# Performance work log

Measured on AMD Instinct MI355X. Metric: run time of the kernel, lower is better.

The kernel has to match this reference:

```python
import jax, jax.numpy as jnp
import numpy as np

T, H, E, I, SI, TOP_K = 4096, 2048, 16, 1024, 4096, 1


def setup_inputs() -> dict:
    key = jax.random.key(0)
    ks = jax.random.split(key, 8)
    s_h = 1.0 / np.sqrt(H)
    s_i = 1.0 / np.sqrt(I)
    s_si = 1.0 / np.sqrt(SI)
    return {
        "hidden_states": jax.random.normal(ks[0], (T, H), jnp.float32),
        "router_w": jax.random.normal(ks[1], (E, H), jnp.float32) * s_h,
        "w_gate": jax.random.normal(ks[2], (E, H, I), jnp.float32) * s_h,
        "w_up": jax.random.normal(ks[3], (E, H, I), jnp.float32) * s_h,
        "w_down": jax.random.normal(ks[4], (E, I, H), jnp.float32) * s_i,
        "ws_gate": jax.random.normal(ks[5], (H, SI), jnp.float32) * s_h,
        "ws_up": jax.random.normal(ks[6], (H, SI), jnp.float32) * s_h,
        "ws_down": jax.random.normal(ks[7], (SI, H), jnp.float32) * s_si,
    }


def reference(hidden_states, router_w, w_gate, w_up, w_down, ws_gate, ws_up, ws_down):
    x = hidden_states  # [T, H]
    # Router: logits -> top-k -> sigmoid weights (Llama4RenormalizeMoeRoutingMethod)
    logits = jnp.einsum("th,eh->te", x, router_w)              # [T, E]
    top_vals, top_idx = jax.lax.top_k(logits, TOP_K)            # [T, K]
    weights = jax.nn.sigmoid(top_vals)                          # [T, K]
    # dispatch[t, e] = router weight if expert e selected for token t, else 0
    onehot = jax.nn.one_hot(top_idx, E, dtype=x.dtype)          # [T, K, E]
    dispatch = jnp.einsum("tke,tk->te", onehot, weights)        # [T, E]
    # Routed experts: router weight applied on input (commutes through the
    # linear gate/up projections as a per-(t,e) scalar applied before SiLU).
    g = jnp.einsum("th,ehi->tei", x, w_gate) * dispatch[:, :, None]  # [T, E, I]
    u = jnp.einsum("th,ehi->tei", x, w_up) * dispatch[:, :, None]    # [T, E, I]
    act = jax.nn.silu(g) * u                                          # [T, E, I]
    # Unselected experts contribute exactly 0 (act==0 there), so summing over
    # E in the down projection is the combine step.
    routed = jnp.einsum("tei,eih->th", act, w_down)             # [T, H]
    # Shared expert (SiLU-gated MLP on the unscaled hidden states)
    shared = (jax.nn.silu(x @ ws_gate) * (x @ ws_up)) @ ws_down  # [T, H]
    return shared + routed
```

## Files before the change

kernel.cpp:

```cpp
#include <hip/hip_runtime.h>
#include <hip/hip_bf16.h>

typedef unsigned short u16;
typedef unsigned int   u32;
typedef __attribute__((ext_vector_type(8))) short short8;
typedef __attribute__((ext_vector_type(4))) float f32x4;

#define T_TOK 4096
#define HDIM  2048
#define NEXP  16
#define IDIM  1024
#define SIDIM 4096
#define RCAP  6144
#define NTIL  48

#define O_WT      0u
#define O_EIDX    16384u
#define O_CNT     32768u
#define O_POS     32832u
#define O_PADOFF  32896u
#define O_TILEEXP 33024u
#define O_TOKROW  33280u
#define O_XBF     65536u
#define O_XSC     (O_XBF + 2u*T_TOK*HDIM)
#define O_ACTS    (O_XSC + 2u*RCAP*HDIM)
#define O_ACTR    (O_ACTS + 2u*T_TOK*SIDIM)

__device__ __forceinline__ u16 f2b(float f) {
  u32 u = __float_as_uint(f);
  u = (u + 0x7FFFu + ((u >> 16) & 1u)) >> 16;
  return (u16)u;
}

__global__ __launch_bounds__(256) void router_k(
    const float* __restrict__ x, const float* __restrict__ rw,
    float* __restrict__ wt, int* __restrict__ eidx, int* __restrict__ cnt) {
  int w = threadIdx.x >> 6, l = threadIdx.x & 63;
  int t = blockIdx.x * 4 + w;
  double acc[NEXP];
#pragma unroll
  for (int e = 0; e < NEXP; ++e) acc[e] = 0.0;
  const float* xp = x + (size_t)t * HDIM;
  for (int hb = 0; hb < HDIM; hb += 256) {
    float4 xv = *(const float4*)(xp + hb + l * 4);
#pragma unroll
    for (int e = 0; e < NEXP; ++e) {
      float4 wv = *(const float4*)(rw + (size_t)e * HDIM + hb + l * 4);
      acc[e] += (double)xv.x * wv.x + (double)xv.y * wv.y
              + (double)xv.z * wv.z + (double)xv.w * wv.w;
    }
  }
#pragma unroll
  for (int e = 0; e < NEXP; ++e) {
    double v = acc[e];
#pragma unroll
    for (int off = 32; off; off >>= 1) v += __shfl_xor(v, off, 64);
    acc[e] = v;
  }
  if (l == 0) {
    double best = acc[0]; int be = 0;
#pragma unroll
    for (int e = 1; e < NEXP; ++e) if (acc[e] > best) { best = acc[e]; be = e; }
    wt[t] = 1.0f / (1.0f + __expf(-(float)best));
    eidx[t] = be;
    atomicAdd(&cnt[be], 1);
  }
}

__global__ void scan_k(const int* __restrict__ cnt, int* __restrict__ pad_off,
                       int* __restrict__ tile_exp, int* __restrict__ pos,
                       int* __restrict__ tok_row) {
  if (threadIdx.x == 0) {
    for (int i = 0; i < 64; ++i) tile_exp[i] = -1;
    int run = 0;
    for (int e = 0; e < NEXP; ++e) {
      pad_off[e] = run;
      int pc = ((cnt[e] + 127) >> 7) << 7;
      for (int tt = run >> 7; tt < (run + pc) >> 7; ++tt) tile_exp[tt] = e;
      run += pc;
      pos[e] = 0;
    }
    pad_off[NEXP] = run;
  }
  for (int i = threadIdx.x; i < RCAP; i += 256) tok_row[i] = -1;
}

__global__ void assign_k(const int* __restrict__ eidx, const int* __restrict__ pad_off,
                         int* __restrict__ pos, int* __restrict__ tok_row) {
  int t = blockIdx.x * 256 + threadIdx.x;
  if (t >= T_TOK) return;
  int e = eidx[t];
  int r = atomicAdd(&pos[e], 1);
  tok_row[pad_off[e] + r] = t;
}

__global__ __launch_bounds__(256) void cvt_k(
    const float* __restrict__ x, const float* __restrict__ wt,
    const int* __restrict__ tok_row, u16* __restrict__ xbf, u16* __restrict__ xsc) {
  int row = blockIdx.x;
  int tid = threadIdx.x;
  if (row < T_TOK) {
    const float* src = x + (size_t)row * HDIM;
    u16* dst = xbf + (size_t)row * HDIM;
#pragma unroll
    for (int i = 0; i < 2; ++i) {
      int c = i * 1024 + tid * 4;
      float4 v = *(const float4*)(src + c);
      uint2 o;
      o.x = (u32)f2b(v.x) | ((u32)f2b(v.y) << 16);
      o.y = (u32)f2b(v.z) | ((u32)f2b(v.w) << 16);
      *(uint2*)(dst + c) = o;
    }
  } else {
    int g = row - T_TOK;
    u16* dst = xsc + (size_t)g * HDIM;
    int t = tok_row[g];
    if (t < 0) {
      uint2 z; z.x = 0u; z.y = 0u;
#pragma unroll
      for (int i = 0; i < 2; ++i) *(uint2*)(dst + i * 1024 + tid * 4) = z;
    } else {
      float s = wt[t];
      const float* src = x + (size_t)t * HDIM;
#pragma unroll
      for (int i = 0; i < 2; ++i) {
        int c = i * 1024 + tid * 4;
        float4 v = *(const float4*)(src + c);
        uint2 o;
        o.x = (u32)f2b(v.x * s) | ((u32)f2b(v.y * s) << 16);
        o.y = (u32)f2b(v.z * s) | ((u32)f2b(v.w * s) << 16);
        *(uint2*)(dst + c) = o;
      }
    }
  }
}


template<bool ROUTED>
__global__ __launch_bounds__(256) void gemm_gu(
    const u16* __restrict__ A, int lda,
    const float* __restrict__ Bg0, const float* __restrict__ Bu0, int ldb,
    int K, u16* __restrict__ act, int ldact,
    const int* __restrict__ tile_exp) {
  __shared__ __align__(16) u16 As[128 * 64];
  __shared__ __align__(16) u16 Bgs[64 * 72];
  __shared__ __align__(16) u16 Bus[64 * 72];
  const int tid = threadIdx.x;
  const int w = tid >> 6, l = tid & 63;
  const int wm = w >> 1, wn = w & 1;
  const int m0 = blockIdx.y * 128, n0 = blockIdx.x * 64;
  const float* Bg = Bg0;
  const float* Bu = Bu0;
  if (ROUTED) {
    int e = tile_exp[blockIdx.y];
    if (e < 0) return;
    size_t off = (size_t)e * (size_t)K * (size_t)ldb;
    Bg += off; Bu += off;
  }
  f32x4 accg[4][2], accu[4][2];
#pragma unroll
  for (int i = 0; i < 4; ++i)
#pragma unroll
    for (int j = 0; j < 2; ++j)
#pragma unroll
      for (int r = 0; r < 4; ++r) { accg[i][j][r] = 0.0f; accu[i][j][r] = 0.0f; }

  const int ra = tid >> 3;
  const int ca = (tid & 7) * 8;
  const u16* Ab = A + (size_t)m0 * lda;

  for (int k0 = 0; k0 < K; k0 += 64) {
    __syncthreads();
#pragma unroll
    for (int i = 0; i < 4; ++i) {
      int r = ra + 32 * i;
      int4 v = *(const int4*)(Ab + (size_t)r * lda + k0 + ca);
      *(int4*)&As[r * 64 + (ca ^ ((r & 7) * 8))] = v;
    }
    {
      const float* bp = Bg + (size_t)(k0 + w * 16) * ldb + n0 + l;
      u16 h[16];
#pragma unroll
      for (int i = 0; i < 16; ++i) h[i] = f2b(bp[(size_t)i * ldb]);
#pragma unroll
      for (int j = 0; j < 4; ++j) {
        uint2 v; v.x = (u32)h[4*j] | ((u32)h[4*j+1] << 16);
        v.y = (u32)h[4*j+2] | ((u32)h[4*j+3] << 16);
        *(uint2*)&Bgs[l * 72 + w * 16 + j * 4] = v;
      }
      bp = Bu + (size_t)(k0 + w * 16) * ldb + n0 + l;
#pragma unroll
      for (int i = 0; i < 16; ++i) h[i] = f2b(bp[(size_t)i * ldb]);
#pragma unroll
      for (int j = 0; j < 4; ++j) {
        uint2 v; v.x = (u32)h[4*j] | ((u32)h[4*j+1] << 16);
        v.y = (u32)h[4*j+2] | ((u32)h[4*j+3] << 16);
        *(uint2*)&Bus[l * 72 + w * 16 + j * 4] = v;
      }
    }
    __syncthreads();
#pragma unroll
    for (int kh = 0; kh < 2; ++kh) {
      short8 af[4];
#pragma unroll
      for (int mf = 0; mf < 4; ++mf) {
        int r = wm * 64 + mf * 16 + (l & 15);
        int c = (kh * 32 + (l >> 4) * 8) ^ ((r & 7) * 8);
        af[mf] = *(const short8*)&As[r * 64 + c];
      }
      short8 bgf[2], buf2[2];
#pragma unroll
      for (int nf = 0; nf < 2; ++nf) {
        int n = wn * 32 + nf * 16 + (l & 15);
        int c = kh * 32 + (l >> 4) * 8;
        bgf[nf]  = *(const short8*)&Bgs[n * 72 + c];
        buf2[nf] = *(const short8*)&Bus[n * 72 + c];
      }
#pragma unroll
      for (int mf = 0; mf < 4; ++mf)
#pragma unroll
        for (int nf = 0; nf < 2; ++nf) {
          accg[mf][nf] = __builtin_amdgcn_mfma_f32_16x16x32_bf16(af[mf], bgf[nf],  accg[mf][nf], 0, 0, 0);
          accu[mf][nf] = __builtin_amdgcn_mfma_f32_16x16x32_bf16(af[mf], buf2[nf], accu[mf][nf], 0, 0, 0);
        }
    }
  }
#pragma unroll
  for (int mf = 0; mf < 4; ++mf)
#pragma unroll
    for (int nf = 0; nf < 2; ++nf) {
      int col = n0 + wn * 32 + nf * 16 + (l & 15);
#pragma unroll
      for (int r = 0; r < 4; ++r) {
        int row = m0 + wm * 64 + mf * 16 + (l >> 4) * 4 + r;
        float g = accg[mf][nf][r], u = accu[mf][nf][r];
        float s = g / (1.0f + __expf(-g));
        act[(size_t)row * ldact + col] = f2b(s * u);
      }
    }
}

template<bool ROUTED>
__global__ __launch_bounds__(256) void gemm_down(
    const u16* __restrict__ A, int lda,
    const float* __restrict__ B0, int ldb, int K,
    float* __restrict__ out, int ldout,
    const int* __restrict__ tile_exp, const int* __restrict__ tok_row) {
  __shared__ __align__(16) u16 As[128 * 64];
  __shared__ __align__(16) u16 Bs[64 * 72];
  const int tid = threadIdx.x;
  const int w = tid >> 6, l = tid & 63;
  const int wm = w >> 1, wn = w & 1;
  const int m0 = blockIdx.y * 128, n0 = blockIdx.x * 64;
  const float* B = B0;
  if (ROUTED) {
    int e = tile_exp[blockIdx.y];
    if (e < 0) return;
    B += (size_t)e * (size_t)K * (size_t)ldb;
  }
  f32x4 acc[4][2];
#pragma unroll
  for (int i = 0; i < 4; ++i)
#pragma unroll
    for (int j = 0; j < 2; ++j)
#pragma unroll
      for (int r = 0; r < 4; ++r) acc[i][j][r] = 0.0f;

  const int ra = tid >> 3;
  const int ca = (tid & 7) * 8;
  const u16* Ab = A + (size_t)m0 * lda;

  for (int k0 = 0; k0 < K; k0 += 64) {
    __syncthreads();
#pragma unroll
    for (int i = 0; i < 4; ++i) {
      int r = ra + 32 * i;
      int4 v = *(const int4*)(Ab + (size_t)r * lda + k0 + ca);
      *(int4*)&As[r * 64 + (ca ^ ((r & 7) * 8))] = v;
    }
    {
      const float* bp = B + (size_t)(k0 + w * 16) * ldb + n0 + l;
      u16 h[16];
#pragma unroll
      for (int i = 0; i < 16; ++i) h[i] = f2b(bp[(size_t)i * ldb]);
#pragma unroll
      for (int j = 0; j < 4; ++j) {
        uint2 v; v.x = (u32)h[4*j] | ((u32)h[4*j+1] << 16);
        v.y = (u32)h[4*j+2] | ((u32)h[4*j+3] << 16);
        *(uint2*)&Bs[l * 72 + w * 16 + j * 4] = v;
      }
    }
    __syncthreads();
#pragma unroll
    for (int kh = 0; kh < 2; ++kh) {
      short8 af[4];
#pragma unroll
      for (int mf = 0; mf < 4; ++mf) {
        int r = wm * 64 + mf * 16 + (l & 15);
        int c = (kh * 32 + (l >> 4) * 8) ^ ((r & 7) * 8);
        af[mf] = *(const short8*)&As[r * 64 + c];
      }
      short8 bf[2];
#pragma unroll
      for (int nf = 0; nf < 2; ++nf) {
        int n = wn * 32 + nf * 16 + (l & 15);
        int c = kh * 32 + (l >> 4) * 8;
        bf[nf] = *(const short8*)&Bs[n * 72 + c];
      }
#pragma unroll
      for (int mf = 0; mf < 4; ++mf)
#pragma unroll
        for (int nf = 0; nf < 2; ++nf)
          acc[mf][nf] = __builtin_amdgcn_mfma_f32_16x16x32_bf16(af[mf], bf[nf], acc[mf][nf], 0, 0, 0);
    }
  }
#pragma unroll
  for (int mf = 0; mf < 4; ++mf)
#pragma unroll
    for (int nf = 0; nf < 2; ++nf) {
      int col = n0 + wn * 32 + nf * 16 + (l & 15);
#pragma unroll
      for (int r = 0; r < 4; ++r) {
        int grow = m0 + wm * 64 + mf * 16 + (l >> 4) * 4 + r;
        float v = acc[mf][nf][r];
        if (ROUTED) {
          int t = tok_row[grow];
          if (t >= 0) out[(size_t)t * ldout + col] += v;
        } else {
          out[(size_t)grow * ldout + col] = v;
        }
      }
    }
}

extern "C" void kernel_launch(void* const* d_in, const int* in_sizes, int n_in,
                              void* d_out, int out_size, void* d_ws, size_t ws_size,
                              hipStream_t stream) {
  const float* x   = (const float*)d_in[0];
  const float* rw  = (const float*)d_in[1];
  const float* wg  = (const float*)d_in[2];
  const float* wu  = (const float*)d_in[3];
  const float* wd  = (const float*)d_in[4];
  const float* wsg = (const float*)d_in[5];
  const float* wsu = (const float*)d_in[6];
  const float* wsd = (const float*)d_in[7];
  float* out = (float*)d_out;
  char* ws = (char*)d_ws;

  float* wt     = (float*)(ws + O_WT);
  int* eidx     = (int*)(ws + O_EIDX);
  int* cnt      = (int*)(ws + O_CNT);
  int* pos      = (int*)(ws + O_POS);
  int* pad_off  = (int*)(ws + O_PADOFF);
  int* tile_exp = (int*)(ws + O_TILEEXP);
  int* tok_row  = (int*)(ws + O_TOKROW);
  u16* xbf      = (u16*)(ws + O_XBF);
  u16* xsc      = (u16*)(ws + O_XSC);
  u16* acts     = (u16*)(ws + O_ACTS);
  u16* actr     = (u16*)(ws + O_ACTR);

  hipMemsetAsync(ws + O_CNT, 0, 128, stream);
  router_k<<<T_TOK / 4, 256, 0, stream>>>(x, rw, wt, eidx, cnt);
  scan_k<<<1, 256, 0, stream>>>(cnt, pad_off, tile_exp, pos, tok_row);
  assign_k<<<T_TOK / 256, 256, 0, stream>>>(eidx, pad_off, pos, tok_row);
  cvt_k<<<T_TOK + RCAP, 256, 0, stream>>>(x, wt, tok_row, xbf, xsc);
  gemm_gu<false><<<dim3(SIDIM / 64, T_TOK / 128), 256, 0, stream>>>(
      xbf, HDIM, wsg, wsu, SIDIM, HDIM, acts, SIDIM, nullptr);
  gemm_gu<true><<<dim3(IDIM / 64, NTIL), 256, 0, stream>>>(
      xsc, HDIM, wg, wu, IDIM, HDIM, actr, IDIM, tile_exp);
  gemm_down<false><<<dim3(HDIM / 64, T_TOK / 128), 256, 0, stream>>>(
      acts, SIDIM, wsd, HDIM, SIDIM, out, HDIM, nullptr, nullptr);
  gemm_down<true><<<dim3(HDIM / 64, NTIL), 256, 0, stream>>>(
      actr, IDIM, wd, HDIM, IDIM, out, HDIM, tile_exp, tok_row);
}
```

Before: 630.5 us.

## Pre-transpose weights to bf16 and rewrite GEMMs with async LDS pipelining

Adds a transpose-convert kernel that turns every fp32 weight matrix into a K-contiguous bf16 copy in workspace on each call. The GEMMs then fetch A and B straight into LDS with global_load_lds and 16-byte loads instead of strided fp32 loads converted in registers. The shared-expert GEMMs move to new 512-thread kernels with 256x128 tiles, double-buffered LDS, barrier-interleaved prefetch, s_setprio around the MFMAs and block-index swizzling. The routed GEMMs use the transposed weights, and the routed down projection gets wider tiles. In exchange, every call re-reads and rewrites all weights, which is extra memory traffic.

After: 649.0 us. 1.03x slower.

```diff
diff --git a/kernel.cpp b/kernel.cpp
--- a/kernel.cpp
+++ b/kernel.cpp
@@ -22,15 +22,28 @@
 #define O_TILEEXP 33024u
 #define O_TOKROW  33280u
 #define O_XBF     65536u
-#define O_XSC     (O_XBF + 2u*T_TOK*HDIM)
-#define O_ACTS    (O_XSC + 2u*RCAP*HDIM)
+#define O_XSC     (O_XBF  + 2u*T_TOK*HDIM)
+#define O_ACTS    (O_XSC  + 2u*RCAP*HDIM)
 #define O_ACTR    (O_ACTS + 2u*T_TOK*SIDIM)
+#define O_WSGT    (O_ACTR + 2u*RCAP*IDIM)
+#define O_WSUT    (O_WSGT + 2u*SIDIM*HDIM)
+#define O_WSDT    (O_WSUT + 2u*SIDIM*HDIM)
+#define O_WGT     (O_WSDT + 2u*HDIM*SIDIM)
+#define O_WUT     (O_WGT  + 2u*NEXP*IDIM*HDIM)
+#define O_WDT     (O_WUT  + 2u*NEXP*IDIM*HDIM)
 
 __device__ __forceinline__ u16 f2b(float f) {
   u32 u = __float_as_uint(f);
   u = (u + 0x7FFFu + ((u >> 16) & 1u)) >> 16;
   return (u16)u;
 }
+
+#define GLDS16(g, l) __builtin_amdgcn_global_load_lds( \
+    (const __attribute__((address_space(1))) void*)(g), \
+    (__attribute__((address_space(3))) void*)(l), 16, 0, 0)
+#define BARX() __builtin_amdgcn_s_barrier()
+#define SETPRIO(x) __builtin_amdgcn_s_setprio(x)
+#define WAITVM(n) asm volatile("s_waitcnt vmcnt(" #n ")" ::: "memory")
 
 __global__ __launch_bounds__(256) void router_k(
     const float* __restrict__ x, const float* __restrict__ rw,
@@ -135,28 +148,243 @@
   }
 }
 
-
-template<bool ROUTED>
-__global__ __launch_bounds__(256) void gemm_gu(
-    const u16* __restrict__ A, int lda,
-    const float* __restrict__ Bg0, const float* __restrict__ Bu0, int ldb,
-    int K, u16* __restrict__ act, int ldact,
-    const int* __restrict__ tile_exp) {
+__global__ __launch_bounds__(256) void tconv_k(
+    const float* __restrict__ src, u16* __restrict__ dst, int K, int N) {
+  __shared__ u32 lt[64][36];
+  size_t boff = (size_t)blockIdx.z * (size_t)K * N;
+  const int n0 = blockIdx.x * 64, k0 = blockIdx.y * 64;
+  const int l = threadIdx.x & 63, w = threadIdx.x >> 6;
+  const float* sp = src + boff + (size_t)(k0 + w * 16) * N + n0 + l;
+  u32 p[8];
+#pragma unroll
+  for (int i = 0; i < 8; ++i) {
+    float a = sp[(size_t)(2 * i) * N];
+    float b = sp[(size_t)(2 * i + 1) * N];
+    p[i] = (u32)f2b(a) | ((u32)f2b(b) << 16);
+  }
+  *(uint4*)&lt[l][w * 8 + 0] = make_uint4(p[0], p[1], p[2], p[3]);
+  *(uint4*)&lt[l][w * 8 + 4] = make_uint4(p[4], p[5], p[6], p[7]);
+  __syncthreads();
+  const int c = threadIdx.x & 7, n2 = threadIdx.x >> 3;
+#pragma unroll
+  for (int rnd = 0; rnd < 2; ++rnd) {
+    int n = n2 + rnd * 32;
+    uint4 v = *(const uint4*)&lt[n][c * 4];
+    *(uint4*)(dst + boff + (size_t)(n0 + n) * K + k0 + c * 8) = v;
+  }
+}
+
+
+__device__ __forceinline__ void mmA(f32x4 (&acc)[4][8], const short8 (&af)[4],
+                                    const short8 (&bfr)[4], int h) {
+  SETPRIO(1);
+#pragma unroll
+  for (int mf = 0; mf < 4; ++mf)
+#pragma unroll
+    for (int nf = 0; nf < 4; ++nf)
+      acc[mf][h * 4 + nf] = __builtin_amdgcn_mfma_f32_16x16x32_bf16(
+          af[mf], bfr[nf], acc[mf][h * 4 + nf], 0, 0, 0);
+  SETPRIO(0);
+}
+__device__ __forceinline__ void mmD(f32x4 (&acc)[4][4], const short8 (&af)[4],
+                                    const short8 (&bfr)[2], int h) {
+  SETPRIO(1);
+#pragma unroll
+  for (int mf = 0; mf < 4; ++mf)
+#pragma unroll
+    for (int nf = 0; nf < 2; ++nf)
+      acc[mf][h * 2 + nf] = __builtin_amdgcn_mfma_f32_16x16x32_bf16(
+          af[mf], bfr[nf], acc[mf][h * 2 + nf], 0, 0, 0);
+  SETPRIO(0);
+}
+
+__global__ __launch_bounds__(512, 2) void gu_sh8(
+    const u16* __restrict__ A, const u16* __restrict__ Bg, const u16* __restrict__ Bu,
+    u16* __restrict__ act) {
+  extern __shared__ u16 sm[];
+  u16* As  = sm;
+  u16* Bsm = sm + 32768;
+  const int bid = blockIdx.x;
+  const int swz = (bid & 7) * 64 + (bid >> 3);
+  const int bx = swz & 31, by = swz >> 5;
+  const int m0 = by * 256, c0 = bx * 128;
+  const int tid = threadIdx.x, l = tid & 63, wid = tid >> 6;
+  const int wm = wid >> 1, wn = wid & 1;
+
+  const int cpos = tid & 3, rr = tid >> 2;
+  const int gc = (cpos ^ (rr & 3)) * 8;
+  const u16* aS0 = A + (size_t)(m0 + rr) * HDIM + gc;
+  const u16* aS1 = A + (size_t)(m0 + 128 + rr) * HDIM + gc;
+  const int mat = (rr >> 6) & 1;
+  const u16* bbase = mat ? Bu : Bg;
+  const u16* bS0 = bbase + (size_t)(c0 + (rr & 63)) * HDIM + gc;
+  const u16* bS1 = bbase + (size_t)(c0 + 64 + (rr & 63)) * HDIM + gc;
+  const int ld0 = tid * 8, ld1 = (512 + tid) * 8;
+
+#define STA_G(bb, kh, koff) do { \
+    GLDS16(aS0 + (koff) + (kh) * 32, As + ((bb) * 2 + (kh)) * 8192 + ld0); \
+    GLDS16(aS1 + (koff) + (kh) * 32, As + ((bb) * 2 + (kh)) * 8192 + ld1); } while (0)
+#define STB_G(bb, kh, koff) do { \
+    GLDS16(bS0 + (koff) + (kh) * 32, Bsm + ((bb) * 2 + (kh)) * 8192 + ld0); \
+    GLDS16(bS1 + (koff) + (kh) * 32, Bsm + ((bb) * 2 + (kh)) * 8192 + ld1); } while (0)
+
+  const int fch = ((l >> 4) ^ (l & 3)) * 8;
+  int aoff[4], boff[8];
+#pragma unroll
+  for (int mf = 0; mf < 4; ++mf) aoff[mf] = (wm * 64 + mf * 16 + (l & 15)) * 32 + fch;
+#pragma unroll
+  for (int i = 0; i < 8; ++i) {
+    int v = wn * 128 + (i >> 2) * 64 + (i & 3) * 16 + (l & 15);
+    boff[i] = v * 32 + fch;
+  }
+#define LDA_G(bb, kh) do { const u16* s_ = As + ((bb) * 2 + (kh)) * 8192; \
+    af[0] = *(const short8*)(s_ + aoff[0]); af[1] = *(const short8*)(s_ + aoff[1]); \
+    af[2] = *(const short8*)(s_ + aoff[2]); af[3] = *(const short8*)(s_ + aoff[3]); } while (0)
+#define LDB_G(bb, kh, h) do { const u16* s_ = Bsm + ((bb) * 2 + (kh)) * 8192; \
+    bfr[0] = *(const short8*)(s_ + boff[(h) * 4 + 0]); bfr[1] = *(const short8*)(s_ + boff[(h) * 4 + 1]); \
+    bfr[2] = *(const short8*)(s_ + boff[(h) * 4 + 2]); bfr[3] = *(const short8*)(s_ + boff[(h) * 4 + 3]); } while (0)
+
+  f32x4 acc[4][8];
+#pragma unroll
+  for (int i = 0; i < 4; ++i)
+#pragma unroll
+    for (int j = 0; j < 8; ++j)
+#pragma unroll
+      for (int r = 0; r < 4; ++r) acc[i][j][r] = 0.0f;
+  short8 af[4], bfr[4];
+
+  STA_G(0, 0, 0); STB_G(0, 0, 0); STA_G(0, 1, 0); STB_G(0, 1, 0);
+  WAITVM(0); BARX();
+  const int NT = HDIM / 64;
+  for (int t = 0; t < NT - 1; ++t) {
+    const int b = t & 1, nb = b ^ 1, kn = (t + 1) * 64;
+    LDA_G(b, 0); LDB_G(b, 0, 0); STA_G(nb, 0, kn); BARX(); mmA(acc, af, bfr, 0); BARX();
+    LDB_G(b, 0, 1);              STB_G(nb, 0, kn); BARX(); mmA(acc, af, bfr, 1); WAITVM(4); BARX();
+    LDA_G(b, 1); LDB_G(b, 1, 0); STA_G(nb, 1, kn); BARX(); mmA(acc, af, bfr, 0); BARX();
+    LDB_G(b, 1, 1);              STB_G(nb, 1, kn); BARX(); mmA(acc, af, bfr, 1); WAITVM(4); BARX();
+  }
+  { const int b = (NT - 1) & 1;
+    LDA_G(b, 0); LDB_G(b, 0, 0); BARX(); mmA(acc, af, bfr, 0); BARX();
+    LDB_G(b, 0, 1);              BARX(); mmA(acc, af, bfr, 1); WAITVM(0); BARX();
+    LDA_G(b, 1); LDB_G(b, 1, 0); BARX(); mmA(acc, af, bfr, 0); BARX();
+    LDB_G(b, 1, 1);              mmA(acc, af, bfr, 1);
+  }
+#pragma unroll
+  for (int mf = 0; mf < 4; ++mf)
+#pragma unroll
+    for (int nf = 0; nf < 4; ++nf) {
+      int col = c0 + wn * 64 + nf * 16 + (l & 15);
+      int rowb = m0 + wm * 64 + mf * 16 + (l >> 4) * 4;
+#pragma unroll
+      for (int r = 0; r < 4; ++r) {
+        float g = acc[mf][nf][r], u = acc[mf][4 + nf][r];
+        float s = g / (1.0f + __expf(-g));
+        act[(size_t)(rowb + r) * SIDIM + col] = f2b(s * u);
+      }
+    }
+#undef STA_G
+#undef STB_G
+#undef LDA_G
+#undef LDB_G
+}
+
+__global__ __launch_bounds__(512, 2) void dn_sh8(
+    const u16* __restrict__ A, const u16* __restrict__ B, float* __restrict__ out) {
+  extern __shared__ u16 sm[];
+  u16* As  = sm;
+  u16* Bsm = sm + 32768;
+  const int bid = blockIdx.x;
+  const int swz = (bid & 7) * 32 + (bid >> 3);
+  const int bx = swz & 15, by = swz >> 4;
+  const int m0 = by * 256, c0 = bx * 128;
+  const int tid = threadIdx.x, l = tid & 63, wid = tid >> 6;
+  const int wm = wid >> 1, wn = wid & 1;
+
+  const int cpos = tid & 3, rr = tid >> 2;
+  const int gc = (cpos ^ (rr & 3)) * 8;
+  const u16* aS0 = A + (size_t)(m0 + rr) * SIDIM + gc;
+  const u16* aS1 = A + (size_t)(m0 + 128 + rr) * SIDIM + gc;
+  const u16* bS  = B + (size_t)(c0 + rr) * SIDIM + gc;
+  const int ld0 = tid * 8, ld1 = (512 + tid) * 8;
+
+#define STA_D(bb, kh, koff) do { \
+    GLDS16(aS0 + (koff) + (kh) * 32, As + ((bb) * 2 + (kh)) * 8192 + ld0); \
+    GLDS16(aS1 + (koff) + (kh) * 32, As + ((bb) * 2 + (kh)) * 8192 + ld1); } while (0)
+#define STB_D(bb, kh, koff) \
+    GLDS16(bS + (koff) + (kh) * 32, Bsm + ((bb) * 2 + (kh)) * 4096 + ld0)
+
+  const int fch = ((l >> 4) ^ (l & 3)) * 8;
+  int aoff[4], boff[4];
+#pragma unroll
+  for (int mf = 0; mf < 4; ++mf) aoff[mf] = (wm * 64 + mf * 16 + (l & 15)) * 32 + fch;
+#pragma unroll
+  for (int i = 0; i < 4; ++i) {
+    int v = wn * 64 + (i >> 1) * 32 + (i & 1) * 16 + (l & 15);
+    boff[i] = v * 32 + fch;
+  }
+#define LDA_D(bb, kh) do { const u16* s_ = As + ((bb) * 2 + (kh)) * 8192; \
+    af[0] = *(const short8*)(s_ + aoff[0]); af[1] = *(const short8*)(s_ + aoff[1]); \
+    af[2] = *(const short8*)(s_ + aoff[2]); af[3] = *(const short8*)(s_ + aoff[3]); } while (0)
+#define LDB_D(bb, kh, h) do { const u16* s_ = Bsm + ((bb) * 2 + (kh)) * 4096; \
+    bfr[0] = *(const short8*)(s_ + boff[(h) * 2 + 0]); \
+    bfr[1] = *(const short8*)(s_ + boff[(h) * 2 + 1]); } while (0)
+
+  f32x4 acc[4][4];
+#pragma unroll
+  for (int i = 0; i < 4; ++i)
+#pragma unroll
+    for (int j = 0; j < 4; ++j)
+#pragma unroll
+      for (int r = 0; r < 4; ++r) acc[i][j][r] = 0.0f;
+  short8 af[4]; short8 bfr[2];
+
+  STA_D(0, 0, 0); STB_D(0, 0, 0); STA_D(0, 1, 0); STB_D(0, 1, 0);
+  WAITVM(0); BARX();
+  const int NT = SIDIM / 64;
+  for (int t = 0; t < NT - 1; ++t) {
+    const int b = t & 1, nb = b ^ 1, kn = (t + 1) * 64;
+    LDA_D(b, 0); LDB_D(b, 0, 0); STA_D(nb, 0, kn); BARX(); mmD(acc, af, bfr, 0); BARX();
+    LDB_D(b, 0, 1);              STB_D(nb, 0, kn); BARX(); mmD(acc, af, bfr, 1); WAITVM(3); BARX();
+    LDA_D(b, 1); LDB_D(b, 1, 0); STA_D(nb, 1, kn); BARX(); mmD(acc, af, bfr, 0); BARX();
+    LDB_D(b, 1, 1);              STB_D(nb, 1, kn); BARX(); mmD(acc, af, bfr, 1); WAITVM(3); BARX();
+  }
+  { const int b = (NT - 1) & 1;
+    LDA_D(b, 0); LDB_D(b, 0, 0); BARX(); mmD(acc, af, bfr, 0); BARX();
+    LDB_D(b, 0, 1);              BARX(); mmD(acc, af, bfr, 1); WAITVM(0); BARX();
+    LDA_D(b, 1); LDB_D(b, 1, 0); BARX(); mmD(acc, af, bfr, 0); BARX();
+    LDB_D(b, 1, 1);              mmD(acc, af, bfr, 1);
+  }
+#pragma unroll
+  for (int mf = 0; mf < 4; ++mf)
+#pragma unroll
+    for (int nf = 0; nf < 4; ++nf) {
+      int col = c0 + wn * 64 + (nf >> 1) * 32 + (nf & 1) * 16 + (l & 15);
+      int rowb = m0 + wm * 64 + mf * 16 + (l >> 4) * 4;
+#pragma unroll
+      for (int r = 0; r < 4; ++r)
+        out[(size_t)(rowb + r) * HDIM + col] = acc[mf][nf][r];
+    }
+#undef STA_D
+#undef STB_D
+#undef LDA_D
+#undef LDB_D
+}
+
+__global__ __launch_bounds__(256) void gu_r(
+    const u16* __restrict__ A, const u16* __restrict__ BgT, const u16* __restrict__ BuT,
+    u16* __restrict__ act, const int* __restrict__ tile_exp) {
   __shared__ __align__(16) u16 As[128 * 64];
-  __shared__ __align__(16) u16 Bgs[64 * 72];
-  __shared__ __align__(16) u16 Bus[64 * 72];
+  __shared__ __align__(16) u16 Bgs[64 * 64];
+  __shared__ __align__(16) u16 Bus[64 * 64];
   const int tid = threadIdx.x;
-  const int w = tid >> 6, l = tid & 63;
+  const int l = tid & 63, w = tid >> 6;
   const int wm = w >> 1, wn = w & 1;
   const int m0 = blockIdx.y * 128, n0 = blockIdx.x * 64;
-  const float* Bg = Bg0;
-  const float* Bu = Bu0;
-  if (ROUTED) {
-    int e = tile_exp[blockIdx.y];
-    if (e < 0) return;
-    size_t off = (size_t)e * (size_t)K * (size_t)ldb;
-    Bg += off; Bu += off;
-  }
+  int e = tile_exp[blockIdx.y];
+  if (e < 0) return;
+  size_t eo = (size_t)e * IDIM * HDIM;
+  const u16* Bg = BgT + eo + (size_t)n0 * HDIM;
+  const u16* Bu = BuT + eo + (size_t)n0 * HDIM;
   f32x4 accg[4][2], accu[4][2];
 #pragma unroll
   for (int i = 0; i < 4; ++i)
@@ -164,57 +392,38 @@
     for (int j = 0; j < 2; ++j)
 #pragma unroll
       for (int r = 0; r < 4; ++r) { accg[i][j][r] = 0.0f; accu[i][j][r] = 0.0f; }
-
-  const int ra = tid >> 3;
-  const int ca = (tid & 7) * 8;
-  const u16* Ab = A + (size_t)m0 * lda;
-
-  for (int k0 = 0; k0 < K; k0 += 64) {
+  const u16* Ab = A + (size_t)m0 * HDIM;
+
+  for (int k0 = 0; k0 < HDIM; k0 += 64) {
     __syncthreads();
 #pragma unroll
-    for (int i = 0; i < 4; ++i) {
-      int r = ra + 32 * i;
-      int4 v = *(const int4*)(Ab + (size_t)r * lda + k0 + ca);
-      *(int4*)&As[r * 64 + (ca ^ ((r & 7) * 8))] = v;
-    }
-    {
-      const float* bp = Bg + (size_t)(k0 + w * 16) * ldb + n0 + l;
-      u16 h[16];
-#pragma unroll
-      for (int i = 0; i < 16; ++i) h[i] = f2b(bp[(size_t)i * ldb]);
-#pragma unroll
-      for (int j = 0; j < 4; ++j) {
-        uint2 v; v.x = (u32)h[4*j] | ((u32)h[4*j+1] << 16);
-        v.y = (u32)h[4*j+2] | ((u32)h[4*j+3] << 16);
-        *(uint2*)&Bgs[l * 72 + w * 16 + j * 4] = v;
-      }
-      bp = Bu + (size_t)(k0 + w * 16) * ldb + n0 + l;
-#pragma unroll
-      for (int i = 0; i < 16; ++i) h[i] = f2b(bp[(size_t)i * ldb]);
-#pragma unroll
-      for (int j = 0; j < 4; ++j) {
-        uint2 v; v.x = (u32)h[4*j] | ((u32)h[4*j+1] << 16);
-        v.y = (u32)h[4*j+2] | ((u32)h[4*j+3] << 16);
-        *(uint2*)&Bus[l * 72 + w * 16 + j * 4] = v;
-      }
+    for (int j = 0; j < 4; ++j) {
+      int c = j * 256 + tid, r = c >> 3, cc = c & 7;
+      GLDS16(Ab + (size_t)r * HDIM + k0 + ((cc ^ (r & 7)) * 8), &As[c * 8]);
+    }
+#pragma unroll
+    for (int j = 0; j < 2; ++j) {
+      int c = j * 256 + tid, r = c >> 3, cc = c & 7;
+      int sc = (cc ^ (r & 7)) * 8;
+      GLDS16(Bg + (size_t)r * HDIM + k0 + sc, &Bgs[c * 8]);
+      GLDS16(Bu + (size_t)r * HDIM + k0 + sc, &Bus[c * 8]);
     }
     __syncthreads();
 #pragma unroll
     for (int kh = 0; kh < 2; ++kh) {
+      const int q = kh * 4 + (l >> 4);
       short8 af[4];
 #pragma unroll
       for (int mf = 0; mf < 4; ++mf) {
         int r = wm * 64 + mf * 16 + (l & 15);
-        int c = (kh * 32 + (l >> 4) * 8) ^ ((r & 7) * 8);
-        af[mf] = *(const short8*)&As[r * 64 + c];
+        af[mf] = *(const short8*)&As[r * 64 + ((q ^ (r & 7)) * 8)];
       }
       short8 bgf[2], buf2[2];
 #pragma unroll
       for (int nf = 0; nf < 2; ++nf) {
         int n = wn * 32 + nf * 16 + (l & 15);
-        int c = kh * 32 + (l >> 4) * 8;
-        bgf[nf]  = *(const short8*)&Bgs[n * 72 + c];
-        buf2[nf] = *(const short8*)&Bus[n * 72 + c];
+        bgf[nf]  = *(const short8*)&Bgs[n * 64 + ((q ^ (n & 7)) * 8)];
+        buf2[nf] = *(const short8*)&Bus[n * 64 + ((q ^ (n & 7)) * 8)];
       }
 #pragma unroll
       for (int mf = 0; mf < 4; ++mf)
@@ -235,100 +444,77 @@
         int row = m0 + wm * 64 + mf * 16 + (l >> 4) * 4 + r;
         float g = accg[mf][nf][r], u = accu[mf][nf][r];
         float s = g / (1.0f + __expf(-g));
-        act[(size_t)row * ldact + col] = f2b(s * u);
-      }
-    }
-}
-
-template<bool ROUTED>
-__global__ __launch_bounds__(256) void gemm_down(
-    const u16* __restrict__ A, int lda,
-    const float* __restrict__ B0, int ldb, int K,
-    float* __restrict__ out, int ldout,
+        act[(size_t)row * IDIM + col] = f2b(s * u);
+      }
+    }
+}
+
+__global__ __launch_bounds__(256) void dn_r(
+    const u16* __restrict__ A, const u16* __restrict__ BT, float* __restrict__ out,
     const int* __restrict__ tile_exp, const int* __restrict__ tok_row) {
   __shared__ __align__(16) u16 As[128 * 64];
-  __shared__ __align__(16) u16 Bs[64 * 72];
+  __shared__ __align__(16) u16 Bs[128 * 64];
   const int tid = threadIdx.x;
-  const int w = tid >> 6, l = tid & 63;
+  const int l = tid & 63, w = tid >> 6;
   const int wm = w >> 1, wn = w & 1;
-  const int m0 = blockIdx.y * 128, n0 = blockIdx.x * 64;
-  const float* B = B0;
-  if (ROUTED) {
-    int e = tile_exp[blockIdx.y];
-    if (e < 0) return;
-    B += (size_t)e * (size_t)K * (size_t)ldb;
-  }
-  f32x4 acc[4][2];
+  const int m0 = blockIdx.y * 128, n0 = blockIdx.x * 128;
+  int e = tile_exp[blockIdx.y];
+  if (e < 0) return;
+  const u16* B = BT + (size_t)e * HDIM * IDIM + (size_t)n0 * IDIM;
+  f32x4 acc[4][4];
 #pragma unroll
   for (int i = 0; i < 4; ++i)
 #pragma unroll
-    for (int j = 0; j < 2; ++j)
+    for (int j = 0; j < 4; ++j)
 #pragma unroll
       for (int r = 0; r < 4; ++r) acc[i][j][r] = 0.0f;
-
-  const int ra = tid >> 3;
-  const int ca = (tid & 7) * 8;
-  const u16* Ab = A + (size_t)m0 * lda;
-
-  for (int k0 = 0; k0 < K; k0 += 64) {
+  const u16* Ab = A + (size_t)m0 * IDIM;
+
+  for (int k0 = 0; k0 < IDIM; k0 += 64) {
     __syncthreads();
 #pragma unroll
-    for (int i = 0; i < 4; ++i) {
-      int r = ra + 32 * i;
-      int4 v = *(const int4*)(Ab + (size_t)r * lda + k0 + ca);
-      *(int4*)&As[r * 64 + (ca ^ ((r & 7) * 8))] = v;
-    }
-    {
-      const float* bp = B + (size_t)(k0 + w * 16) * ldb + n0 + l;
-      u16 h[16];
-#pragma unroll
-      for (int i = 0; i < 16; ++i) h[i] = f2b(bp[(size_t)i * ldb]);
-#pragma unroll
-      for (int j = 0; j < 4; ++j) {
-        uint2 v; v.x = (u32)h[4*j] | ((u32)h[4*j+1] << 16);
-        v.y = (u32)h[4*j+2] | ((u32)h[4*j+3] << 16);
-        *(uint2*)&Bs[l * 72 + w * 16 + j * 4] = v;
-      }
+    for (int j = 0; j < 4; ++j) {
+      int c = j * 256 + tid, r = c >> 3, cc = c & 7;
+      GLDS16(Ab + (size_t)r * IDIM + k0 + ((cc ^ (r & 7)) * 8), &As[c * 8]);
+    }
+#pragma unroll
+    for (int j = 0; j < 4; ++j) {
+      int c = j * 256 + tid, r = c >> 3, cc = c & 7;
+      GLDS16(B + (size_t)r * IDIM + k0 + ((cc ^ (r & 7)) * 8), &Bs[c * 8]);
     }
     __syncthreads();
 #pragma unroll
     for (int kh = 0; kh < 2; ++kh) {
+      const int q = kh * 4 + (l >> 4);
       short8 af[4];
 #pragma unroll
       for (int mf = 0; mf < 4; ++mf) {
         int r = wm * 64 + mf * 16 + (l & 15);
-        int c = (kh * 32 + (l >> 4) * 8) ^ ((r & 7) * 8);
-        af[mf] = *(const short8*)&As[r * 64 + c];
-      }
-      short8 bf[2];
-#pragma unroll
-      for (int nf = 0; nf < 2; ++nf) {
-        int n = wn * 32 + nf * 16 + (l & 15);
-        int c = kh * 32 + (l >> 4) * 8;
-        bf[nf] = *(const short8*)&Bs[n * 72 + c];
+        af[mf] = *(const short8*)&As[r * 64 + ((q ^ (r & 7)) * 8)];
+      }
+      short8 bf[4];
+#pragma unroll
+      for (int nf = 0; nf < 4; ++nf) {
+        int n = wn * 64 + nf * 16 + (l & 15);
+        bf[nf] = *(const short8*)&Bs[n * 64 + ((q ^ (n & 7)) * 8)];
       }
 #pragma unroll
       for (int mf = 0; mf < 4; ++mf)
 #pragma unroll
-        for (int nf = 0; nf < 2; ++nf)
+        for (int nf = 0; nf < 4; ++nf)
           acc[mf][nf] = __builtin_amdgcn_mfma_f32_16x16x32_bf16(af[mf], bf[nf], acc[mf][nf], 0, 0, 0);
     }
   }
 #pragma unroll
   for (int mf = 0; mf < 4; ++mf)
 #pragma unroll
-    for (int nf = 0; nf < 2; ++nf) {
-      int col = n0 + wn * 32 + nf * 16 + (l & 15);
+    for (int nf = 0; nf < 4; ++nf) {
+      int col = n0 + wn * 64 + nf * 16 + (l & 15);
 #pragma unroll
       for (int r = 0; r < 4; ++r) {
         int grow = m0 + wm * 64 + mf * 16 + (l >> 4) * 4 + r;
-        float v = acc[mf][nf][r];
-        if (ROUTED) {
-          int t = tok_row[grow];
-          if (t >= 0) out[(size_t)t * ldout + col] += v;
-        } else {
-          out[(size_t)grow * ldout + col] = v;
-        }
+        int t = tok_row[grow];
+        if (t >= 0) out[(size_t)t * HDIM + col] += acc[mf][nf][r];
       }
     }
 }
@@ -358,18 +544,34 @@
   u16* xsc      = (u16*)(ws + O_XSC);
   u16* acts     = (u16*)(ws + O_ACTS);
   u16* actr     = (u16*)(ws + O_ACTR);
+  u16* wsgT     = (u16*)(ws + O_WSGT);
+  u16* wsuT     = (u16*)(ws + O_WSUT);
+  u16* wsdT     = (u16*)(ws + O_WSDT);
+  u16* wgT      = (u16*)(ws + O_WGT);
+  u16* wuT      = (u16*)(ws + O_WUT);
+  u16* wdT      = (u16*)(ws + O_WDT);
 
   hipMemsetAsync(ws + O_CNT, 0, 128, stream);
+  tconv_k<<<dim3(SIDIM / 64, HDIM / 64, 1), 256, 0, stream>>>(wsg, wsgT, HDIM, SIDIM);
+  tconv_k<<<dim3(SIDIM / 64, HDIM / 64, 1), 256, 0, stream>>>(wsu, wsuT, HDIM, SIDIM);
+  tconv_k<<<dim3(HDIM / 64, SIDIM / 64, 1), 256, 0, stream>>>(wsd, wsdT, SIDIM, HDIM);
+  tconv_k<<<dim3(IDIM / 64, HDIM / 64, NEXP), 256, 0, stream>>>(wg, wgT, HDIM, IDIM);
+  tconv_k<<<dim3(IDIM / 64, HDIM / 64, NEXP), 256, 0, stream>>>(wu, wuT, HDIM, IDIM);
+  tconv_k<<<dim3(HDIM / 64, IDIM / 64, NEXP), 256, 0, stream>>>(wd, wdT, IDIM, HDIM);
+
   router_k<<<T_TOK / 4, 256, 0, stream>>>(x, rw, wt, eidx, cnt);
   scan_k<<<1, 256, 0, stream>>>(cnt, pad_off, tile_exp, pos, tok_row);
   assign_k<<<T_TOK / 256, 256, 0, stream>>>(eidx, pad_off, pos, tok_row);
   cvt_k<<<T_TOK + RCAP, 256, 0, stream>>>(x, wt, tok_row, xbf, xsc);
-  gemm_gu<false><<<dim3(SIDIM / 64, T_TOK / 128), 256, 0, stream>>>(
-      xbf, HDIM, wsg, wsu, SIDIM, HDIM, acts, SIDIM, nullptr);
-  gemm_gu<true><<<dim3(IDIM / 64, NTIL), 256, 0, stream>>>(
-      xsc, HDIM, wg, wu, IDIM, HDIM, actr, IDIM, tile_exp);
-  gemm_down<false><<<dim3(HDIM / 64, T_TOK / 128), 256, 0, stream>>>(
-      acts, SIDIM, wsd, HDIM, SIDIM, out, HDIM, nullptr, nullptr);
-  gemm_down<true><<<dim3(HDIM / 64, NTIL), 256, 0, stream>>>(
-      actr, IDIM, wd, HDIM, IDIM, out, HDIM, tile_exp, tok_row);
-}
+
+  static bool attr_set = false;
+  if (!attr_set) {
+    hipFuncSetAttribute((const void*)gu_sh8, hipFuncAttributeMaxDynamicSharedMemorySize, 131072);
+    hipFuncSetAttribute((const void*)dn_sh8, hipFuncAttributeMaxDynamicSharedMemorySize, 98304);
+    attr_set = true;
+  }
+  gu_sh8<<<512, 512, 131072, stream>>>(xbf, wsgT, wsuT, acts);
+  gu_r<<<dim3(IDIM / 64, NTIL), 256, 0, stream>>>(xsc, wgT, wuT, actr, tile_exp);
+  dn_sh8<<<256, 512, 98304, stream>>>(acts, wsdT, out);
+  dn_r<<<dim3(HDIM / 128, NTIL), 256, 0, stream>>>(actr, wdT, out, tile_exp, tok_row);
+}
```
